# Performance work log

Hardware: AMD Instinct MI355X
Metric: run time of the kernel (lower is better)

The kernel has to match this reference:

```python
import jax, jax.numpy as jnp
import numpy as np

T_SYN = 201
SYN_BASIS_NO = 3


def setup_inputs() -> dict:
    key = jax.random.key(0)
    ks = jax.random.split(key, 5)
    T_data, n_e, n_i, sub_no, B = 100000, 500, 200, 20, SYN_BASIS_NO
    S_e = jax.random.uniform(ks[0], (T_data, n_e), jnp.float32)
    S_i = jax.random.uniform(ks[1], (T_data, n_i), jnp.float32)
    C_syn_e = jax.random.uniform(ks[2], (sub_no, n_e), jnp.float32)
    C_syn_i = jax.random.uniform(ks[3], (sub_no, n_i), jnp.float32)
    # init values from the torch module
    K_syn = jnp.concatenate([jnp.full((sub_no, B, 1), 0.02, jnp.float32),
                             jnp.full((sub_no, B, 1), -0.02, jnp.float32)], axis=-1)
    tau_syn = jnp.tile(jnp.arange(1.6, 1.6 + B, dtype=jnp.float32).reshape(-1, 1), (1, 2))
    delta_syn = 2.0 * jax.random.uniform(ks[4], (sub_no, 2), jnp.float32)
    return dict(S_e=S_e, S_i=S_i, C_syn_e=C_syn_e, C_syn_i=C_syn_i,
                K_syn=K_syn, tau_syn=tau_syn, delta_syn=delta_syn)


def _kernels(K_syn, tau_syn, delta_syn):
    # Vectorized alpha-function kernel bank: [sub_no, 2(e/i), T_syn]
    t = jnp.arange(T_SYN, dtype=jnp.float32)                     # [T]
    ts = t[None, None, :] - delta_syn[:, :, None]                # [S,2,T]
    ts = jnp.where(ts < 0.0, 0.0, ts)                            # clamp like t[t<0]=0
    tau = jnp.exp(tau_syn)                                       # [B,2]
    tt = ts[:, None, :, :] / tau[None, :, :, None]               # [S,B,2,T]
    basis = tt * jnp.exp(-tt)                                    # alpha functions
    return jnp.einsum('sbct,sbc->sct', basis, K_syn)             # [S,2,T]


def _causal_conv(x, kern):
    # x: [T_data, S]; kern: [S, T_syn]; out[t,s] = sum_k kern[s,k] * x[t-k,s]
    S = x.shape[1]
    lhs = x.T[None]                          # [1,S,T_data]
    rhs = kern[:, ::-1][:, None, :]          # flip -> lax correlation == causal conv
    out = jax.lax.conv_general_dilated(lhs, rhs, (1,), [(T_SYN - 1, 0)],
                                       feature_group_count=S,
                                       dimension_numbers=('NCH', 'OIH', 'NCH'))
    return out[0].T                          # [T_data, S]


def reference(S_e, S_i, C_syn_e, C_syn_i, K_syn, tau_syn, delta_syn):
    kern = _kernels(K_syn, tau_syn, delta_syn)   # [S,2,T_syn]
    in_e = S_e @ C_syn_e.T                       # [T_data, sub_no]
    in_i = S_i @ C_syn_i.T                       # [T_data, sub_no]
    return _causal_conv(in_e, kern[:, 0]) + _causal_conv(in_i, kern[:, 1])
```

## Files before the change

### kernel.cpp

```cpp
#include <hip/hip_runtime.h>
#include <hip/hip_bf16.h>

#define TDATA 100000
#define NE 500
#define NI 200
#define SUB 20
#define NB 3
#define TSYN 201

#define SROW 100552
#define HROW 216
#define NSTEP_E 32
#define NSTEP_I 13
#define NF4_E 4000
#define NF4_I 1600
#define NTILE 3125

#define OFF_HP  0
#define OFF_BE  8640
#define OFF_BI  (OFF_BE + 8192)
#define OFF_INT (OFF_BI + 3584)

typedef __bf16 bf16x8 __attribute__((ext_vector_type(8)));
typedef __bf16 bf16x4 __attribute__((ext_vector_type(4)));
typedef float  f32x16 __attribute__((ext_vector_type(16)));

__global__ __launch_bounds__(256) void setup_kernel(
    const float* __restrict__ C_e, const float* __restrict__ C_i,
    const float* __restrict__ K_syn, const float* __restrict__ tau_syn,
    const float* __restrict__ delta_syn, float* __restrict__ ws)
{
    int idx = blockIdx.x * 256 + threadIdx.x;
    if (idx < 8640) {
        int c = idx / (SUB * HROW);
        int rem = idx - c * (SUB * HROW);
        int s = rem / HROW;
        int k = (rem - s * HROW) - 8;
        float v = 0.f;
        if (k >= 0 && k < TSYN) {
            float ts = (float)k - delta_syn[s * 2 + c];
            ts = ts < 0.f ? 0.f : ts;
            #pragma unroll
            for (int b = 0; b < NB; b++) {
                float tt = ts / expf(tau_syn[b * 2 + c]);
                v += K_syn[(s * NB + b) * 2 + c] * tt * expf(-tt);
            }
        }
        ws[OFF_HP + idx] = v;
    } else if (idx < 30720) {
        int j = idx - 8640;
        const int PERROW = 552;
        int row = j / PERROW;
        int e = j - row * PERROW;
        int off = (e < 200) ? e : (200 + TDATA + (e - 200));
        ws[OFF_INT + (long)row * SROW + off] = 0.f;
    } else if (idx < 47104) {
        int j = idx - 30720;
        int step = j >> 9;
        int lane = (j >> 3) & 63;
        int jj = j & 7;
        int k = step * 16 + ((lane >> 5) << 3) + jj;
        int s = lane & 31;
        float v = (s < SUB && k < NE) ? C_e[s * NE + k] : 0.f;
        ((__hip_bfloat16*)(ws + OFF_BE))[j] = (__hip_bfloat16)v;
    } else {
        int j = idx - 47104;
        int step = j >> 9;
        int lane = (j >> 3) & 63;
        int jj = j & 7;
        int k = step * 16 + ((lane >> 5) << 3) + jj;
        int s = lane & 31;
        float v = (s < SUB && k < NI) ? C_i[s * NI + k] : 0.f;
        ((__hip_bfloat16*)(ws + OFF_BI))[j] = (__hip_bfloat16)v;
    }
}

template<int K, int NSTEP, int NF4, int RB>
__device__ __forceinline__ void gemm9_body(
    const float* __restrict__ S, const float* __restrict__ wsA,
    float* __restrict__ inT, unsigned char* smem, int blk, int tid)
{
    constexpr int NJ   = (NF4 + 511) / 512;
    constexpr int NAQ  = (NSTEP + 7) / 8;
    constexpr int F4R  = K / 4;
    constexpr int TB8  = (16 * NSTEP * 2 - 2 * K) / 8;
    const int lane = tid & 63, wave = tid >> 6;

    const float4* src = (const float4*)(S + (long)blk * (32 * K));
#define IDX9(J)  (tid + 512 * (J))
#define CIDX9(J) (IDX9(J) < NF4 ? IDX9(J) : NF4 - 1)
    float4 va = src[CIDX9(0)];
    float4 vb = src[CIDX9(1)];
    float4 vc = src[CIDX9(2)];
    float4 vd = src[CIDX9(3)];
    float4 ve, vf, vg, vh;
    if constexpr (NJ == 8) {
        ve = src[CIDX9(4)];
        vf = src[CIDX9(5)];
        vg = src[CIDX9(6)];
        vh = src[CIDX9(7)];
    }

    if (tid < 32 * TB8) {
        int r = tid / TB8, p = tid - r * TB8;
        int byt = (r * RB + 2 * K + 8 * p) ^ ((r & 7) << 4);
        *(unsigned long long*)(smem + byt) = 0ull;
    }

#define STG9(J, V) {                                                        \
    int idx = IDX9(J);                                                      \
    if ((J) < NJ - 1 || idx < NF4) {                                        \
        int r = idx / F4R;                                                  \
        int c4 = idx - r * F4R;                                             \
        int byt = (r * RB + c4 * 8) ^ ((r & 7) << 4);                       \
        bf16x4 bv;                                                          \
        bv[0] = (__bf16)V.x; bv[1] = (__bf16)V.y;                           \
        bv[2] = (__bf16)V.z; bv[3] = (__bf16)V.w;                           \
        *(bf16x4*)(smem + byt) = bv;                                        \
    }                                                                       \
}
    STG9(0, va); STG9(1, vb); STG9(2, vc); STG9(3, vd);
    if constexpr (NJ == 8) {
        STG9(4, ve); STG9(5, vf); STG9(6, vg); STG9(7, vh);
    }
#undef STG9
#undef IDX9
#undef CIDX9

    const bf16x8* afr = (const bf16x8*)wsA;
    bf16x8 A[NAQ];
    #pragma unroll
    for (int q = 0; q < NAQ; q++) {
        int u = wave + 8 * q;
        if (u < NSTEP) A[q] = afr[u * 64 + lane];
    }
    __syncthreads();

    const int n = lane & 31, h = lane >> 5;
    f32x16 acc = {};
    #pragma unroll
    for (int q = 0; q < NAQ; q++) {
        int u = wave + 8 * q;
        if (u < NSTEP) {
            int byt = (n * RB + 16 * (2 * u + h)) ^ ((n & 7) << 4);
            bf16x8 b = *(const bf16x8*)(smem + byt);
            acc = __builtin_amdgcn_mfma_f32_32x32x16_bf16(A[q], b, acc, 0, 0, 0);
        }
    }

    __syncthreads();
    float* scr = (float*)smem;
    if (wave != 0) {
        float4* dst = (float4*)(scr + ((wave - 1) * 64 + lane) * 16);
        dst[0] = make_float4(acc[0],  acc[1],  acc[2],  acc[3]);
        dst[1] = make_float4(acc[4],  acc[5],  acc[6],  acc[7]);
        dst[2] = make_float4(acc[8],  acc[9],  acc[10], acc[11]);
        dst[3] = make_float4(acc[12], acc[13], acc[14], acc[15]);
    }
    __syncthreads();
    if (wave == 0) {
        #pragma unroll
        for (int w = 0; w < 7; w++) {
            const float4* s4 = (const float4*)(scr + (w * 64 + lane) * 16);
            float4 p0 = s4[0], p1 = s4[1], p2 = s4[2], p3 = s4[3];
            acc[0]  += p0.x; acc[1]  += p0.y; acc[2]  += p0.z; acc[3]  += p0.w;
            acc[4]  += p1.x; acc[5]  += p1.y; acc[6]  += p1.z; acc[7]  += p1.w;
            acc[8]  += p2.x; acc[9]  += p2.y; acc[10] += p2.z; acc[11] += p2.w;
            acc[12] += p3.x; acc[13] += p3.y; acc[14] += p3.z; acc[15] += p3.w;
        }
        const long t = (long)blk * 32 + n;
        #pragma unroll
        for (int r = 0; r < 16; r++) {
            int m = (r & 3) + 8 * (r >> 2) + 4 * h;
            if (m < SUB)
                inT[(long)m * SROW + 200 + t] = acc[r];
        }
    }
}

__global__ __launch_bounds__(512) void gemm_kernel(
    const float* __restrict__ Se, const float* __restrict__ Si,
    float* __restrict__ ws)
{
    __shared__ __align__(16) unsigned char smem[32768];
    const int tid = threadIdx.x;
    if (!(blockIdx.x & 1))
        gemm9_body<NE, NSTEP_E, NF4_E, 1024>(Se, ws + OFF_BE, ws + OFF_INT,
                                             smem, blockIdx.x >> 1, tid);
    else
        gemm9_body<NI, NSTEP_I, NF4_I, 512>(Si, ws + OFF_BI,
                                            ws + OFF_INT + (long)SUB * SROW,
                                            smem, blockIdx.x >> 1, tid);
}

#define SW(i) ((i) + ((i) >> 5))

__global__ __launch_bounds__(256) void conv_kernel(
    const float* __restrict__ ws, float* __restrict__ out)
{
    __shared__ __align__(16) float W[2][2336];
    __shared__ __align__(16) float HT[2][208];
    const int tid = threadIdx.x;
    const int s = blockIdx.y;
    const long t0 = (long)blockIdx.x * 2048;

    for (int i = tid; i < 1128; i += 256) {
        int c = i >= 564;
        int i4 = i - c * 564;
        float4 v = *(const float4*)(ws + OFF_INT + (long)(c * SUB + s) * SROW
                                    + t0 - 8 + 4 * i4);
        int b = 4 * i4;
        int p = SW(b);
        W[c][p] = v.x; W[c][p + 1] = v.y; W[c][p + 2] = v.z; W[c][p + 3] = v.w;
    }
    if (tid < 104) {
        int c = tid >= 52;
        int j4 = (tid - c * 52) * 4;
        *(float4*)&HT[c][j4] =
            *(const float4*)(ws + OFF_HP + (c * SUB + s) * HROW + 8 + j4);
    }
    __syncthreads();

    float acc[8];
    #pragma unroll
    for (int r = 0; r < 8; r++) acc[r] = 0.f;

    #pragma unroll
    for (int c = 0; c < 2; c++) {
        #pragma unroll 2
        for (int g = 0; g < 26; g++) {
            int k0 = g << 3;
            int xb = (tid << 3) + 200 - k0;
            float x[16];
            #pragma unroll
            for (int q = 0; q < 16; q++) x[q] = W[c][SW(xb + q)];
            float h[8];
            *(float4*)&h[0] = *(const float4*)&HT[c][k0];
            *(float4*)&h[4] = *(const float4*)&HT[c][k0 + 4];
            #pragma unroll
            for (int j = 0; j < 8; j++)
                #pragma unroll
                for (int r = 0; r < 8; r++)
                    acc[r] += h[j] * x[8 + r - j];
        }
    }

    #pragma unroll
    for (int r = 0; r < 8; r++) {
        long t = t0 + 8 * tid + r;
        if (t < TDATA) out[t * SUB + s] = acc[r];
    }
}

extern "C" void kernel_launch(void* const* d_in, const int* in_sizes, int n_in,
                              void* d_out, int out_size, void* d_ws, size_t ws_size,
                              hipStream_t stream)
{
    const float* S_e     = (const float*)d_in[0];
    const float* S_i     = (const float*)d_in[1];
    const float* C_e     = (const float*)d_in[2];
    const float* C_i     = (const float*)d_in[3];
    const float* K_syn   = (const float*)d_in[4];
    const float* tau_syn = (const float*)d_in[5];
    const float* delta   = (const float*)d_in[6];
    float* out = (float*)d_out;
    float* ws  = (float*)d_ws;

    hipLaunchKernelGGL(setup_kernel, dim3(212), dim3(256), 0, stream,
                       C_e, C_i, K_syn, tau_syn, delta, ws);
    hipLaunchKernelGGL(gemm_kernel, dim3(2 * NTILE), dim3(512), 0, stream,
                       S_e, S_i, ws);
    hipLaunchKernelGGL(conv_kernel, dim3(49, SUB), dim3(256), 0, stream,
                       ws, out);
}
```

Measured before the change: 392.6 us.

## Make GEMM kernel persistent with register prefetch of next tile and split reduction

Replaces the one-tile-per-block GEMM launch with a persistent grid of 512 blocks, split between the excitatory and inhibitory inputs, that loop over tiles. Each block prefetches the next tile's global loads into registers while the MFMAs for the current tile run. The cross-wave reduction now uses a separate swizzled scratch region and is spread across all eight waves instead of being done by wave 0 alone. This is meant to hide global load latency and remove the per-block launch and serialized reduction cost, at the price of doubling shared memory to 64 KB and depending on a fixed block-count split between the two inputs.

```diff
diff --git a/kernel.cpp b/kernel.cpp
--- a/kernel.cpp
+++ b/kernel.cpp
@@ -15,6 +15,8 @@
 #define NF4_E 4000
 #define NF4_I 1600
 #define NTILE 3125
+#define NBE 366
+#define NBI 146
 
 #define OFF_HP  0
 #define OFF_BE  8640
@@ -76,29 +78,24 @@
 }
 
 template<int K, int NSTEP, int NF4, int RB>
-__device__ __forceinline__ void gemm9_body(
+__device__ __forceinline__ void gemm10_body(
     const float* __restrict__ S, const float* __restrict__ wsA,
-    float* __restrict__ inT, unsigned char* smem, int blk, int tid)
-{
-    constexpr int NJ   = (NF4 + 511) / 512;
-    constexpr int NAQ  = (NSTEP + 7) / 8;
-    constexpr int F4R  = K / 4;
-    constexpr int TB8  = (16 * NSTEP * 2 - 2 * K) / 8;
+    float* __restrict__ inT, unsigned char* smem, int bid, int nbl, int tid)
+{
+    constexpr int NJ  = (NF4 + 511) / 512;
+    constexpr int NAQ = (NSTEP + 7) / 8;
+    constexpr int F4R = K / 4;
+    constexpr int TB8 = (16 * NSTEP * 2 - 2 * K) / 8;
     const int lane = tid & 63, wave = tid >> 6;
-
-    const float4* src = (const float4*)(S + (long)blk * (32 * K));
-#define IDX9(J)  (tid + 512 * (J))
-#define CIDX9(J) (IDX9(J) < NF4 ? IDX9(J) : NF4 - 1)
-    float4 va = src[CIDX9(0)];
-    float4 vb = src[CIDX9(1)];
-    float4 vc = src[CIDX9(2)];
-    float4 vd = src[CIDX9(3)];
-    float4 ve, vf, vg, vh;
-    if constexpr (NJ == 8) {
-        ve = src[CIDX9(4)];
-        vf = src[CIDX9(5)];
-        vg = src[CIDX9(6)];
-        vh = src[CIDX9(7)];
+    const int n = lane & 31, h = lane >> 5;
+    float* scr = (float*)(smem + 32768);
+
+    const bf16x8* afr = (const bf16x8*)wsA;
+    bf16x8 A[NAQ];
+    #pragma unroll
+    for (int q = 0; q < NAQ; q++) {
+        int u = wave + 8 * q;
+        if (u < NSTEP) A[q] = afr[u * 64 + lane];
     }
 
     if (tid < 32 * TB8) {
@@ -107,8 +104,22 @@
         *(unsigned long long*)(smem + byt) = 0ull;
     }
 
-#define STG9(J, V) {                                                        \
-    int idx = IDX9(J);                                                      \
+    int g = bid;
+    const float4* src = (const float4*)(S + (long)g * (32 * K));
+    float4 va, vb, vc, vd, ve, vf, vg, vh;
+
+#define IDX10(J)  (tid + 512 * (J))
+#define CI10(J)   (IDX10(J) < NF4 ? IDX10(J) : NF4 - 1)
+#define GLD10() do {                                                        \
+    va = src[CI10(0)]; vb = src[CI10(1)];                                   \
+    vc = src[CI10(2)]; vd = src[CI10(3)];                                   \
+    if constexpr (NJ == 8) {                                                \
+        ve = src[CI10(4)]; vf = src[CI10(5)];                               \
+        vg = src[CI10(6)]; vh = src[CI10(7)];                               \
+    }                                                                       \
+} while (0)
+#define STG10(J, V) {                                                       \
+    int idx = IDX10(J);                                                     \
     if ((J) < NJ - 1 || idx < NF4) {                                        \
         int r = idx / F4R;                                                  \
         int c4 = idx - r * F4R;                                             \
@@ -119,78 +130,82 @@
         *(bf16x4*)(smem + byt) = bv;                                        \
     }                                                                       \
 }
-    STG9(0, va); STG9(1, vb); STG9(2, vc); STG9(3, vd);
-    if constexpr (NJ == 8) {
-        STG9(4, ve); STG9(5, vf); STG9(6, vg); STG9(7, vh);
-    }
-#undef STG9
-#undef IDX9
-#undef CIDX9
-
-    const bf16x8* afr = (const bf16x8*)wsA;
-    bf16x8 A[NAQ];
-    #pragma unroll
-    for (int q = 0; q < NAQ; q++) {
-        int u = wave + 8 * q;
-        if (u < NSTEP) A[q] = afr[u * 64 + lane];
-    }
-    __syncthreads();
-
-    const int n = lane & 31, h = lane >> 5;
-    f32x16 acc = {};
-    #pragma unroll
-    for (int q = 0; q < NAQ; q++) {
-        int u = wave + 8 * q;
-        if (u < NSTEP) {
-            int byt = (n * RB + 16 * (2 * u + h)) ^ ((n & 7) << 4);
-            bf16x8 b = *(const bf16x8*)(smem + byt);
-            acc = __builtin_amdgcn_mfma_f32_32x32x16_bf16(A[q], b, acc, 0, 0, 0);
-        }
-    }
-
-    __syncthreads();
-    float* scr = (float*)smem;
-    if (wave != 0) {
-        float4* dst = (float4*)(scr + ((wave - 1) * 64 + lane) * 16);
-        dst[0] = make_float4(acc[0],  acc[1],  acc[2],  acc[3]);
-        dst[1] = make_float4(acc[4],  acc[5],  acc[6],  acc[7]);
-        dst[2] = make_float4(acc[8],  acc[9],  acc[10], acc[11]);
-        dst[3] = make_float4(acc[12], acc[13], acc[14], acc[15]);
-    }
-    __syncthreads();
-    if (wave == 0) {
+
+    GLD10();
+
+    for (;;) {
+        STG10(0, va); STG10(1, vb); STG10(2, vc); STG10(3, vd);
+        if constexpr (NJ == 8) {
+            STG10(4, ve); STG10(5, vf); STG10(6, vg); STG10(7, vh);
+        }
+        __syncthreads();
+
+        const int gn = g + nbl;
+        const bool more = gn < NTILE;
+        if (more) {
+            src = (const float4*)(S + (long)gn * (32 * K));
+            GLD10();
+        }
+
+        f32x16 acc = {};
         #pragma unroll
-        for (int w = 0; w < 7; w++) {
-            const float4* s4 = (const float4*)(scr + (w * 64 + lane) * 16);
-            float4 p0 = s4[0], p1 = s4[1], p2 = s4[2], p3 = s4[3];
-            acc[0]  += p0.x; acc[1]  += p0.y; acc[2]  += p0.z; acc[3]  += p0.w;
-            acc[4]  += p1.x; acc[5]  += p1.y; acc[6]  += p1.z; acc[7]  += p1.w;
-            acc[8]  += p2.x; acc[9]  += p2.y; acc[10] += p2.z; acc[11] += p2.w;
-            acc[12] += p3.x; acc[13] += p3.y; acc[14] += p3.z; acc[15] += p3.w;
-        }
-        const long t = (long)blk * 32 + n;
+        for (int q = 0; q < NAQ; q++) {
+            int u = wave + 8 * q;
+            if (u < NSTEP) {
+                int byt = (n * RB + 16 * (2 * u + h)) ^ ((n & 7) << 4);
+                bf16x8 b = *(const bf16x8*)(smem + byt);
+                acc = __builtin_amdgcn_mfma_f32_32x32x16_bf16(A[q], b, acc, 0, 0, 0);
+            }
+        }
+
         #pragma unroll
-        for (int r = 0; r < 16; r++) {
-            int m = (r & 3) + 8 * (r >> 2) + 4 * h;
-            if (m < SUB)
-                inT[(long)m * SROW + 200 + t] = acc[r];
-        }
-    }
-}
-
-__global__ __launch_bounds__(512) void gemm_kernel(
+        for (int q4 = 0; q4 < 4; q4++) {
+            int w0 = ((wave * 64 + lane) * 16 + 4 * q4) ^ ((lane & 7) << 2);
+            *(float4*)(scr + w0) = make_float4(acc[4 * q4],     acc[4 * q4 + 1],
+                                               acc[4 * q4 + 2], acc[4 * q4 + 3]);
+        }
+        __syncthreads();
+
+        {
+            float s0 = 0.f, s1 = 0.f;
+            #pragma unroll
+            for (int p = 0; p < 8; p++) {
+                int wb = (((p * 64 + lane) * 16 + 4 * (wave >> 1))
+                          ^ ((lane & 7) << 2)) + 2 * (wave & 1);
+                float2 v2 = *(const float2*)(scr + wb);
+                s0 += v2.x; s1 += v2.y;
+            }
+            const long t = (long)g * 32 + n;
+            const int r0i = 2 * wave, r1i = 2 * wave + 1;
+            const int m0 = (r0i & 3) + 8 * (r0i >> 2) + 4 * h;
+            const int m1 = (r1i & 3) + 8 * (r1i >> 2) + 4 * h;
+            if (m0 < SUB) inT[(long)m0 * SROW + 200 + t] = s0;
+            if (m1 < SUB) inT[(long)m1 * SROW + 200 + t] = s1;
+        }
+
+        if (!more) break;
+        g = gn;
+    }
+#undef GLD10
+#undef STG10
+#undef IDX10
+#undef CI10
+}
+
+__global__ __launch_bounds__(512, 4) void gemm_kernel(
     const float* __restrict__ Se, const float* __restrict__ Si,
     float* __restrict__ ws)
 {
-    __shared__ __align__(16) unsigned char smem[32768];
+    __shared__ __align__(16) unsigned char smem[65536];
     const int tid = threadIdx.x;
-    if (!(blockIdx.x & 1))
-        gemm9_body<NE, NSTEP_E, NF4_E, 1024>(Se, ws + OFF_BE, ws + OFF_INT,
-                                             smem, blockIdx.x >> 1, tid);
+    const int bid = blockIdx.x;
+    if (bid < NBE)
+        gemm10_body<NE, NSTEP_E, NF4_E, 1024>(Se, ws + OFF_BE, ws + OFF_INT,
+                                              smem, bid, NBE, tid);
     else
-        gemm9_body<NI, NSTEP_I, NF4_I, 512>(Si, ws + OFF_BI,
-                                            ws + OFF_INT + (long)SUB * SROW,
-                                            smem, blockIdx.x >> 1, tid);
+        gemm10_body<NI, NSTEP_I, NF4_I, 512>(Si, ws + OFF_BI,
+                                             ws + OFF_INT + (long)SUB * SROW,
+                                             smem, bid - NBE, NBI, tid);
 }
 
 #define SW(i) ((i) + ((i) >> 5))
@@ -268,7 +283,7 @@
 
     hipLaunchKernelGGL(setup_kernel, dim3(212), dim3(256), 0, stream,
                        C_e, C_i, K_syn, tau_syn, delta, ws);
-    hipLaunchKernelGGL(gemm_kernel, dim3(2 * NTILE), dim3(512), 0, stream,
+    hipLaunchKernelGGL(gemm_kernel, dim3(NBE + NBI), dim3(512), 0, stream,
                        S_e, S_i, ws);
     hipLaunchKernelGGL(conv_kernel, dim3(49, SUB), dim3(256), 0, stream,
                        ws, out);
```

New measurement: 393.0 us. No clear change (+0.1%).
